# Optimization experiments

Measured on AMD Instinct MI355X. Metric: run time of the kernel, lower is better.

## Reference

```python
import jax, jax.numpy as jnp
import numpy as np

B, M, N = 16, 128, 256
USER_DIM, ANT_DIM, EDGE_DIM = 8, 2, 1
HIDDEN, HEADS = 128, 4
HD = HIDDEN // HEADS
WB, DMIN, HZ, PMAX = 2.0, 0.01, 10.0, 1.0
SCALE = 1.0 / float(np.sqrt(HD))
NEG = 0.2  # leaky relu slope


def leaky(x):
    return jnp.where(x >= 0, x, NEG * x)


def ln(x, g, b, eps=1e-5):
    m = jnp.mean(x, axis=-1, keepdims=True)
    v = jnp.mean((x - m) ** 2, axis=-1, keepdims=True)
    return (x - m) * jax.lax.rsqrt(v + eps) * g + b


def setup_inputs() -> dict:
    key = jax.random.key(0)
    ks = jax.random.split(key, 16)
    rn = lambda k, shape, s: jax.random.normal(k, shape, jnp.float32) * s
    inp = {
        "user_feats": jax.random.normal(ks[0], (B, M, USER_DIM), jnp.float32),
        "ant_feats": jax.random.uniform(ks[1], (B, N, ANT_DIM), jnp.float32),
        "edge_feats": jax.random.uniform(ks[2], (B, M, N, EDGE_DIM), jnp.float32),
        # per-head projections (Linear no-bias) + their LayerNorm affine params
        "Wu": rn(ks[3], (HEADS, HD, USER_DIM), 0.5),
        "ln_u_g": jnp.ones((HEADS, HD)), "ln_u_b": jnp.zeros((HEADS, HD)),
        "Wa": rn(ks[4], (HEADS, HD, ANT_DIM), 0.5),
        "ln_a_g": jnp.ones((HEADS, HD)), "ln_a_b": jnp.zeros((HEADS, HD)),
        "We": rn(ks[5], (HEADS, HD, EDGE_DIM), 0.5),
        "ln_e_g": jnp.ones((HEADS, HD)), "ln_e_b": jnp.zeros((HEADS, HD)),
        "attn_v": rn(ks[6], (HEADS, HD), 0.5),
        # residual proj for antennas (the user residual branch is dead code in the block)
        "Wra": rn(ks[7], (HIDDEN, ANT_DIM), 0.5), "bra": jnp.zeros((HIDDEN,)),
        "ln_ant_g": jnp.ones((HIDDEN,)), "ln_ant_b": jnp.zeros((HIDDEN,)),
        # mlp_ant
        "Wm1": rn(ks[8], (HIDDEN // 2, HIDDEN), 0.1), "bm1": jnp.full((HIDDEN // 2,), 0.1),
        "Wm2": rn(ks[9], (2, HIDDEN // 2), 0.1), "bm2": jnp.full((2,), 0.1),
        # readouts over antenna axis
        "Wd1": rn(ks[10], (2 * N, N), 0.05), "bd1": jnp.zeros((2 * N,)),
        "Wd2": rn(ks[11], (N, 2 * N), 0.05), "bd2": jnp.zeros((N,)),
        "Wp1": rn(ks[12], (2 * N, N), 0.05), "bp1": jnp.zeros((2 * N,)),
        "Wp2": rn(ks[13], (N, 2 * N), 0.05), "bp2": jnp.zeros((N,)),
    }
    return inp


def reference(user_feats, ant_feats, edge_feats, Wu, ln_u_g, ln_u_b, Wa, ln_a_g, ln_a_b,
              We, ln_e_g, ln_e_b, attn_v, Wra, bra, ln_ant_g, ln_ant_b,
              Wm1, bm1, Wm2, bm2, Wd1, bd1, Wd2, bd2, Wp1, bp1, Wp2, bp2):
    # --- per-head bipartite attention (all heads batched on axis h) ---
    U = leaky(ln(jnp.einsum('bmi,hdi->hbmd', user_feats, Wu), ln_u_g[:, None, None, :], ln_u_b[:, None, None, :]))  # [h,B,M,hd]
    A = leaky(ln(jnp.einsum('bni,hdi->hbnd', ant_feats, Wa), ln_a_g[:, None, None, :], ln_a_b[:, None, None, :]))   # [h,B,N,hd]
    E = leaky(ln(jnp.einsum('bmni,hdi->hbmnd', edge_feats, We), ln_e_g[:, None, None, None, :], ln_e_b[:, None, None, None, :]))  # [h,B,M,N,hd]
    inter = leaky(U[:, :, :, None, :] + A[:, :, None, :, :] + E)                # [h,B,M,N,hd]
    scores = jnp.einsum('hbmnd,hd->hbmn', inter, attn_v) * SCALE
    alpha = jax.nn.softmax(scores, axis=-1)                                      # max-subtract softmax over N
    ant_out = jnp.einsum('hbmd,hbmn->hbnd', U, alpha)                            # [h,B,N,hd]
    ant_cat = jnp.transpose(ant_out, (1, 2, 0, 3)).reshape(B, N, HIDDEN)         # concat heads
    a_attn = jax.nn.relu(ant_cat + leaky(ant_feats @ Wra.T + bra))
    # --- block readouts ---
    a_attn = ln(a_attn, ln_ant_g, ln_ant_b)
    h1 = jax.nn.relu(a_attn @ Wm1.T + bm1)
    ant2d = jnp.clip(jax.nn.relu(h1 @ Wm2.T + bm2), -200.0, 200.0)               # [B,N,2]
    rd = jax.nn.relu(ant2d[..., 0] @ Wd1.T + bd1) @ Wd2.T + bd2                  # [B,N]
    rp = jax.nn.relu(ant2d[..., 1] @ Wp1.T + bp1) @ Wp2.T + bp2                  # [B,N]
    rd = jnp.clip(rd, 0.0, 100.0)
    rp = jnp.nan_to_num(rp, nan=0.0, posinf=1.0, neginf=0.0)
    # delta path
    Bmax = 2.0 * WB - (N - 1) * DMIN
    da = jax.nn.relu(rd)
    sd = jnp.sum(da, axis=1, keepdims=True)
    sdelta = jnp.clip((Bmax / jnp.maximum(Bmax, sd)) * da, 0.0, 100.0)
    idx = jnp.arange(N, dtype=sdelta.dtype)
    # closed form of the sequential recurrence x[n] = x[n-1] + sdelta[n] + DMIN - WB
    x = jnp.cumsum(sdelta, axis=1) + idx * DMIN - (idx + 1.0) * WB
    positions = jnp.stack([x, jnp.zeros_like(x), jnp.full_like(x, HZ)], axis=-1)  # [B,N,3]
    # power path
    eps = 1e-3
    pa = jnp.clip(jnp.nan_to_num(jax.nn.relu(rp), nan=0.0, posinf=1.0, neginf=0.0), 0.0, 1.0)
    sp = jnp.nan_to_num(jnp.sum(pa, axis=1, keepdims=True), nan=eps, posinf=eps, neginf=-eps)
    denom = jnp.maximum(sp, eps)
    sfp = jax.lax.stop_gradient(jnp.nan_to_num(PMAX / denom, nan=1.0, posinf=1.0, neginf=0.0))
    spow = jnp.clip(jnp.nan_to_num(sfp * pa, nan=0.0, posinf=1.0, neginf=0.0), 0.0, 1.0)
    ant_feats_out = jnp.stack([sdelta, spow], axis=-1)                            # [B,N,2]
    diff = user_feats[..., :2][:, :, None, :] - positions[:, None, :, :2]         # [B,M,N,2]
    edge_feats_new = jnp.sqrt(jnp.sum(diff * diff, axis=-1, keepdims=True))       # [B,M,N,1]
    return (ant_feats_out, edge_feats_new, positions)
```

## Files before the change

### kernel.cpp

```cpp
#include <hip/hip_runtime.h>
#include <math.h>

#define H_   4
#define HD_  32
#define B_   16
#define M_   128
#define N_   256
#define MC_  16
#define MCH_ 8
#define SCALE_ 0.17677669529663687f

__device__ __forceinline__ float lrelu_f(float x) { return x >= 0.f ? x : 0.2f * x; }

__global__ __launch_bounds__(256) void k2_attn(
    const float* __restrict__ uf, const float* __restrict__ af,
    const float* __restrict__ edge,
    const float* __restrict__ Wu, const float* __restrict__ gu, const float* __restrict__ bu,
    const float* __restrict__ Wa, const float* __restrict__ ga, const float* __restrict__ ba,
    const float* __restrict__ We, const float* __restrict__ ge, const float* __restrict__ be,
    const float* __restrict__ av, float* __restrict__ P)
{
  int blk = blockIdx.x;
  int h = blk & 3, b = (blk >> 2) & 15, mc = blk >> 6;
  int tid = threadIdx.x, n = tid;
  int lane = tid & 63, wid = tid >> 6;
  __shared__ float AB[N_ * 33];
  __shared__ float4 Ut4[HD_][2];
  __shared__ float4 cbv[HD_];
  __shared__ float wred[2][MCH_][4];
  __shared__ float vw_s;

  if (tid < 32) {
    int d = tid;
    float w = We[h * HD_ + d];
    float s = w;
    #pragma unroll
    for (int o = 16; o > 0; o >>= 1) s += __shfl_xor(s, o, 32);
    float mw = s * (1.f / 32.f);
    float df = w - mw;
    float v2 = df * df;
    #pragma unroll
    for (int o = 16; o > 0; o >>= 1) v2 += __shfl_xor(v2, o, 32);
    if (d == 0) vw_s = v2 * (1.f / 32.f);
    float vv = av[h * HD_ + d] * SCALE_;
    cbv[d] = make_float4(df * ge[h * HD_ + d], be[h * HD_ + d], 0.6f * vv, 0.4f * vv);
  }
  int m0 = mc * MCH_;
  if (tid < 128) {
    int m_loc = tid >> 4, s = tid & 15, dd = s * 2;
    const float* urow = uf + (size_t)(b * M_ + m0 + m_loc) * 8;
    const float* w0 = Wu + (h * HD_ + dd) * 8;
    float x0 = 0.f, x1 = 0.f;
    #pragma unroll
    for (int i = 0; i < 8; ++i) { float u = urow[i]; x0 = fmaf(u, w0[i], x0); x1 = fmaf(u, w0[8 + i], x1); }
    float sm = x0 + x1;
    #pragma unroll
    for (int o = 8; o > 0; o >>= 1) sm += __shfl_xor(sm, o, 64);
    float mean = sm * (1.f / 32.f);
    float d0 = x0 - mean, d1 = x1 - mean;
    float vv = fmaf(d0, d0, d1 * d1);
    #pragma unroll
    for (int o = 8; o > 0; o >>= 1) vv += __shfl_xor(vv, o, 64);
    float rs = rsqrtf(vv * (1.f / 32.f) + 1e-5f);
    float y0 = fmaf(d0 * rs, gu[h * HD_ + dd],     bu[h * HD_ + dd]);
    float y1 = fmaf(d1 * rs, gu[h * HD_ + dd + 1], bu[h * HD_ + dd + 1]);
    ((float*)Ut4)[dd * MCH_ + m_loc]       = lrelu_f(y0);
    ((float*)Ut4)[(dd + 1) * MCH_ + m_loc] = lrelu_f(y1);
  }
  {
    float a0 = af[(b * N_ + n) * 2 + 0], a1 = af[(b * N_ + n) * 2 + 1];
    float ar[HD_]; float sm = 0.f;
    #pragma unroll
    for (int d = 0; d < HD_; ++d) {
      ar[d] = fmaf(a0, Wa[(h * HD_ + d) * 2], a1 * Wa[(h * HD_ + d) * 2 + 1]);
      sm += ar[d];
    }
    float mean = sm * (1.f / 32.f); float vv = 0.f;
    #pragma unroll
    for (int d = 0; d < HD_; ++d) { ar[d] -= mean; vv = fmaf(ar[d], ar[d], vv); }
    float rs = rsqrtf(vv * (1.f / 32.f) + 1e-5f);
    #pragma unroll
    for (int d = 0; d < HD_; ++d)
      AB[n * 33 + d] = lrelu_f(fmaf(ar[d] * rs, ga[h * HD_ + d], ba[h * HD_ + d]));
  }
  __syncthreads();
  float vw = vw_s;
  float tm[MCH_];
  #pragma unroll
  for (int mm = 0; mm < MCH_; ++mm) {
    float e = edge[(size_t)(b * M_ + m0 + mm) * N_ + n];
    tm[mm] = e * rsqrtf(fmaf(e * e, vw, 1e-5f));
  }
  float sc[MCH_];
  #pragma unroll
  for (int mm = 0; mm < MCH_; ++mm) sc[mm] = 0.f;
  const float* arow = &AB[n * 33];
  for (int d = 0; d < HD_; ++d) {
    float ad = arow[d];
    float4 qc = cbv[d];
    float4 u0 = Ut4[d][0], u1 = Ut4[d][1];
#define STEP(mi, uval) { float w_ = fmaf(tm[mi], qc.x, qc.y); \
    float E_ = fmaf(0.4f, fabsf(w_), 0.6f * w_); \
    float x_ = ad + uval + E_; \
    sc[mi] = fmaf(qc.z, x_, fmaf(qc.w, fabsf(x_), sc[mi])); }
    STEP(0, u0.x)  STEP(1, u0.y)  STEP(2, u0.z)  STEP(3, u0.w)
    STEP(4, u1.x)  STEP(5, u1.y)  STEP(6, u1.z)  STEP(7, u1.w)
#undef STEP
  }
  #pragma unroll
  for (int mm = 0; mm < MCH_; ++mm) {
    float v = sc[mm];
    #pragma unroll
    for (int o = 32; o > 0; o >>= 1) v = fmaxf(v, __shfl_xor(v, o, 64));
    if (lane == 0) wred[0][mm][wid] = v;
  }
  __syncthreads();
  #pragma unroll
  for (int mm = 0; mm < MCH_; ++mm) {
    float mx = fmaxf(fmaxf(wred[0][mm][0], wred[0][mm][1]),
                     fmaxf(wred[0][mm][2], wred[0][mm][3]));
    float em = __expf(sc[mm] - mx);
    sc[mm] = em;
    float ss = em;
    #pragma unroll
    for (int o = 32; o > 0; o >>= 1) ss += __shfl_xor(ss, o, 64);
    if (lane == 0) wred[1][mm][wid] = ss;
  }
  __syncthreads();
  #pragma unroll
  for (int mm = 0; mm < MCH_; ++mm) {
    float tot = (wred[1][mm][0] + wred[1][mm][1]) + (wred[1][mm][2] + wred[1][mm][3]);
    sc[mm] = sc[mm] / tot;
  }
  __syncthreads();
  float* accr = &AB[n * 33];
  for (int d = 0; d < HD_; ++d) {
    float4 u0 = Ut4[d][0], u1 = Ut4[d][1];
    float a0 = 0.f;
    a0 = fmaf(sc[0], u0.x, a0);  a0 = fmaf(sc[1], u0.y, a0);
    a0 = fmaf(sc[2], u0.z, a0);  a0 = fmaf(sc[3], u0.w, a0);
    a0 = fmaf(sc[4], u1.x, a0);  a0 = fmaf(sc[5], u1.y, a0);
    a0 = fmaf(sc[6], u1.z, a0);  a0 = fmaf(sc[7], u1.w, a0);
    accr[d] = a0;
  }
  __syncthreads();
  float* Pbase = P + (size_t)((mc * 4 + h) * B_ + b) * (N_ * HD_);
  for (int i = tid; i < N_ * HD_; i += 256) {
    int nn = i >> 5, d = i & 31;
    Pbase[i] = AB[nn * 33 + d];
  }
}

__global__ __launch_bounds__(256) void k3_mlp(
    const float* __restrict__ P, const float* __restrict__ af,
    const float* __restrict__ Wra, const float* __restrict__ bra,
    const float* __restrict__ gant, const float* __restrict__ bant,
    const float* __restrict__ Wm1, const float* __restrict__ bm1,
    const float* __restrict__ Wm2, const float* __restrict__ bm2,
    float* __restrict__ rd_in, float* __restrict__ rp_in)
{
  int b = blockIdx.x >> 4, nt = blockIdx.x & 15;
  int tid = threadIdx.x;
  int n_loc = tid >> 4, s = tid & 15;
  int n = nt * 16 + n_loc;
  int jj0 = s * 8;
  int hh = s >> 2, d0 = (s & 3) * 8;
  __shared__ float Wm1s[64][128];
  __shared__ float a2s[16][128];
  __shared__ float h1s[16][64];

  {
    const float4* wg = (const float4*)Wm1;
    float4* wl = (float4*)Wm1s;
    #pragma unroll
    for (int k = 0; k < 8; ++k) wl[tid + 256 * k] = wg[tid + 256 * k];
  }
  float cat[8];
  #pragma unroll
  for (int k = 0; k < 8; ++k) cat[k] = 0.f;
  #pragma unroll
  for (int mc = 0; mc < MC_; ++mc) {
    const float* base = P + (size_t)((mc * 4 + hh) * B_ + b) * (N_ * HD_) + n * HD_ + d0;
    float4 p0 = ((const float4*)base)[0], p1 = ((const float4*)base)[1];
    cat[0] += p0.x; cat[1] += p0.y; cat[2] += p0.z; cat[3] += p0.w;
    cat[4] += p1.x; cat[5] += p1.y; cat[6] += p1.z; cat[7] += p1.w;
  }
  float af0 = af[(b * N_ + n) * 2 + 0], af1 = af[(b * N_ + n) * 2 + 1];
  float a1[8]; float sm = 0.f;
  #pragma unroll
  for (int k = 0; k < 8; ++k) {
    int jj = jj0 + k;
    float r = fmaf(Wra[jj * 2], af0, fmaf(Wra[jj * 2 + 1], af1, bra[jj]));
    a1[k] = fmaxf(cat[k] + lrelu_f(r), 0.f);
    sm += a1[k];
  }
  #pragma unroll
  for (int o = 8; o > 0; o >>= 1) sm += __shfl_xor(sm, o, 64);
  float mean = sm * (1.f / 128.f);
  float vv = 0.f;
  #pragma unroll
  for (int k = 0; k < 8; ++k) { a1[k] -= mean; vv = fmaf(a1[k], a1[k], vv); }
  #pragma unroll
  for (int o = 8; o > 0; o >>= 1) vv += __shfl_xor(vv, o, 64);
  float rs = rsqrtf(vv * (1.f / 128.f) + 1e-5f);
  #pragma unroll
  for (int k = 0; k < 8; ++k) {
    int jj = jj0 + k;
    a2s[n_loc][jj] = fmaf(a1[k] * rs, gant[jj], bant[jj]);
  }
  __syncthreads();
  #pragma unroll
  for (int k = 0; k < 4; ++k) {
    int o = tid + 256 * k;
    int row = o & 63, nl = o >> 6;
    const float4* wr = (const float4*)Wm1s[row];
    const float4* xr = (const float4*)a2s[nl];
    float c0 = 0.f, c1 = 0.f, c2 = 0.f, c3 = 0.f;
    #pragma unroll
    for (int c = 0; c < 32; ++c) {
      int cc = (c + row) & 31;
      float4 w = wr[cc], x = xr[cc];
      c0 = fmaf(w.x, x.x, c0); c1 = fmaf(w.y, x.y, c1);
      c2 = fmaf(w.z, x.z, c2); c3 = fmaf(w.w, x.w, c3);
    }
    h1s[nl][row] = fmaxf((c0 + c1) + (c2 + c3) + bm1[row], 0.f);
  }
  __syncthreads();
  {
    int c = s >> 3, e0 = (s & 7) * 8;
    float p = 0.f;
    #pragma unroll
    for (int k = 0; k < 8; ++k) p = fmaf(h1s[n_loc][e0 + k], Wm2[c * 64 + e0 + k], p);
    #pragma unroll
    for (int o = 4; o > 0; o >>= 1) p += __shfl_xor(p, o, 64);
    if ((s & 7) == 0) {
      float v = p + bm2[c];
      v = fminf(fmaxf(v, 0.f), 200.f);
      (c == 0 ? rd_in : rp_in)[b * N_ + n] = v;
    }
  }
}

__global__ __launch_bounds__(256) void k4a_l1(
    const float* __restrict__ rd_in, const float* __restrict__ rp_in,
    const float* __restrict__ Wd1, const float* __restrict__ bd1,
    const float* __restrict__ Wp1, const float* __restrict__ bp1,
    float* __restrict__ d1buf)
{
  int r = blockIdx.x * 4 + (threadIdx.x >> 6);
  int lane = threadIdx.x & 63;
  int path = r >> 13;
  int rem = r & 8191;
  int b = rem >> 9, i = rem & 511;
  const float* W = (path ? Wp1 : Wd1) + (size_t)i * N_;
  const float* bias = path ? bp1 : bd1;
  const float* x = (path ? rp_in : rd_in) + b * N_;
  float4 w = ((const float4*)W)[lane];
  float4 xv = ((const float4*)x)[lane];
  float s = fmaf(w.x, xv.x, fmaf(w.y, xv.y, fmaf(w.z, xv.z, w.w * xv.w)));
  #pragma unroll
  for (int o = 32; o > 0; o >>= 1) s += __shfl_xor(s, o, 64);
  if (lane == 0) d1buf[r] = fmaxf(s + bias[i], 0.f);
}

__global__ __launch_bounds__(256) void k4b_l2(
    const float* __restrict__ d1buf,
    const float* __restrict__ Wd2, const float* __restrict__ bd2,
    const float* __restrict__ Wp2, const float* __restrict__ bp2,
    float* __restrict__ rdbuf, float* __restrict__ rpbuf)
{
  int r = blockIdx.x * 4 + (threadIdx.x >> 6);
  int lane = threadIdx.x & 63;
  int path = r >> 12;
  int rem = r & 4095;
  int b = rem >> 8, n = rem & 255;
  const float* W = (path ? Wp2 : Wd2) + (size_t)n * (2 * N_);
  const float* x = d1buf + path * (B_ * 2 * N_) + b * (2 * N_);
  float4 w0 = ((const float4*)W)[lane * 2], w1 = ((const float4*)W)[lane * 2 + 1];
  float4 x0 = ((const float4*)x)[lane * 2], x1 = ((const float4*)x)[lane * 2 + 1];
  float s = fmaf(w0.x, x0.x, fmaf(w0.y, x0.y, fmaf(w0.z, x0.z, w0.w * x0.w)));
  s = fmaf(w1.x, x1.x, fmaf(w1.y, x1.y, fmaf(w1.z, x1.z, fmaf(w1.w, x1.w, s))));
  #pragma unroll
  for (int o = 32; o > 0; o >>= 1) s += __shfl_xor(s, o, 64);
  if (lane == 0) {
    if (path == 0) {
      float rd = s + bd2[n];
      rd = fminf(fmaxf(rd, 0.f), 100.f);
      rdbuf[b * N_ + n] = rd;
    } else {
      float rp = s + bp2[n];
      if (isnan(rp)) rp = 0.f;
      else if (isinf(rp)) rp = rp > 0.f ? 1.f : 0.f;
      float pa = fminf(fmaxf(rp, 0.f), 1.f);
      rpbuf[b * N_ + n] = pa;
    }
  }
}

__global__ __launch_bounds__(256) void k4c_final(
    const float* __restrict__ rdbuf, const float* __restrict__ rpbuf,
    const float* __restrict__ uf,
    float* __restrict__ out_af, float* __restrict__ out_pos, float* __restrict__ out_edge)
{
  int b = blockIdx.x >> 4, g = blockIdx.x & 15;
  int q = threadIdx.x;
  int lane = q & 63, wid = q >> 6;
  __shared__ float red[8];
  float rd = rdbuf[b * N_ + q];
  float pa = rpbuf[b * N_ + q];
  float s = rd, s2 = pa;
  #pragma unroll
  for (int o = 32; o > 0; o >>= 1) { s += __shfl_xor(s, o, 64); s2 += __shfl_xor(s2, o, 64); }
  if (lane == 0) { red[wid] = s; red[4 + wid] = s2; }
  __syncthreads();
  float sd = red[0] + red[1] + red[2] + red[3];
  float sp = red[4] + red[5] + red[6] + red[7];
  const float Bmax = 2.f * 2.0f - (N_ - 1) * 0.01f;
  float f = Bmax / fmaxf(Bmax, sd);
  float sdelta = fminf(fmaxf(f * rd, 0.f), 100.f);
  float sfp = 1.0f / fmaxf(sp, 1e-3f);
  float spow = fminf(sfp * pa, 1.f);
  float val = sdelta;
  #pragma unroll
  for (int o = 1; o < 64; o <<= 1) {
    float t = __shfl_up(val, o, 64);
    if (lane >= o) val += t;
  }
  __syncthreads();
  if (lane == 63) red[wid] = val;
  __syncthreads();
  float off = 0.f;
  #pragma unroll
  for (int w2 = 0; w2 < 4; ++w2) if (w2 < wid) off += red[w2];
  float x = val + off + (float)q * 0.01f - (float)(q + 1) * 2.0f;
  if (g == 0) {
    out_af[(b * N_ + q) * 2 + 0] = sdelta;
    out_af[(b * N_ + q) * 2 + 1] = spow;
    out_pos[(b * N_ + q) * 3 + 0] = x;
    out_pos[(b * N_ + q) * 3 + 1] = 0.f;
    out_pos[(b * N_ + q) * 3 + 2] = 10.0f;
  }
  #pragma unroll
  for (int k = 0; k < 8; ++k) {
    int m = g * 8 + k;
    float u0 = uf[(b * M_ + m) * 8 + 0], u1 = uf[(b * M_ + m) * 8 + 1];
    float dx = u0 - x;
    out_edge[(size_t)(b * M_ + m) * N_ + q] = sqrtf(fmaf(dx, dx, u1 * u1));
  }
}

extern "C" void kernel_launch(void* const* d_in, const int* in_sizes, int n_in,
                              void* d_out, int out_size, void* d_ws, size_t ws_size,
                              hipStream_t stream) {
  (void)in_sizes; (void)n_in; (void)out_size; (void)ws_size;
  const float* uf   = (const float*)d_in[0];
  const float* af   = (const float*)d_in[1];
  const float* edge = (const float*)d_in[2];
  const float* Wu   = (const float*)d_in[3];
  const float* gu   = (const float*)d_in[4];
  const float* bu   = (const float*)d_in[5];
  const float* Wa   = (const float*)d_in[6];
  const float* ga   = (const float*)d_in[7];
  const float* ba   = (const float*)d_in[8];
  const float* We   = (const float*)d_in[9];
  const float* ge   = (const float*)d_in[10];
  const float* be   = (const float*)d_in[11];
  const float* av   = (const float*)d_in[12];
  const float* Wra  = (const float*)d_in[13];
  const float* bra  = (const float*)d_in[14];
  const float* gant = (const float*)d_in[15];
  const float* bant = (const float*)d_in[16];
  const float* Wm1  = (const float*)d_in[17];
  const float* bm1  = (const float*)d_in[18];
  const float* Wm2  = (const float*)d_in[19];
  const float* bm2  = (const float*)d_in[20];
  const float* Wd1  = (const float*)d_in[21];
  const float* bd1  = (const float*)d_in[22];
  const float* Wd2  = (const float*)d_in[23];
  const float* bd2  = (const float*)d_in[24];
  const float* Wp1  = (const float*)d_in[25];
  const float* bp1  = (const float*)d_in[26];
  const float* Wp2  = (const float*)d_in[27];
  const float* bp2  = (const float*)d_in[28];

  float* ws    = (float*)d_ws;
  float* P     = ws;
  float* rd_in = ws + 8388608;
  float* rp_in = ws + 8392704;
  float* d1buf = ws + 8396800;
  float* rdbuf = ws + 8413184;
  float* rpbuf = ws + 8417280;

  float* out      = (float*)d_out;
  float* out_af   = out;
  float* out_edge = out + 8192;
  float* out_pos  = out + 532480;

  hipLaunchKernelGGL(k2_attn, dim3(1024), dim3(256), 0, stream,
                     uf, af, edge, Wu, gu, bu, Wa, ga, ba, We, ge, be, av, P);
  hipLaunchKernelGGL(k3_mlp, dim3(256), dim3(256), 0, stream,
                     P, af, Wra, bra, gant, bant, Wm1, bm1, Wm2, bm2, rd_in, rp_in);
  hipLaunchKernelGGL(k4a_l1, dim3(4096), dim3(256), 0, stream,
                     rd_in, rp_in, Wd1, bd1, Wp1, bp1, d1buf);
  hipLaunchKernelGGL(k4b_l2, dim3(2048), dim3(256), 0, stream,
                     d1buf, Wd2, bd2, Wp2, bp2, rdbuf, rpbuf);
  hipLaunchKernelGGL(k4c_final, dim3(256), dim3(256), 0, stream,
                     rdbuf, rpbuf, uf, out_af, out_pos, out_edge);
}
```

Baseline: 170.6 us.

## Use packed fp16 math in attention scoring and store intermediate P as fp16

The attention kernel's score and value-aggregation loops now use packed half2 FMAs, with a partial float accumulation every 8 dims. The per-head partial output buffer P is written and read in fp16 instead of fp32, halving that intermediate traffic between the attention and MLP kernels. Shared memory layouts are reorganized into fp16 arrays. This lowers ALU and memory cost in exchange for reduced precision in the softmax logits and the accumulated outputs.

```diff
diff --git a/kernel.cpp b/kernel.cpp
--- a/kernel.cpp
+++ b/kernel.cpp
@@ -1,4 +1,5 @@
 #include <hip/hip_runtime.h>
+#include <hip/hip_fp16.h>
 #include <math.h>
 
 #define H_   4
@@ -12,21 +13,32 @@
 
 __device__ __forceinline__ float lrelu_f(float x) { return x >= 0.f ? x : 0.2f * x; }
 
+__device__ __forceinline__ __half2 u2h_(unsigned u) {
+  union { unsigned u; __half2 h; } c; c.u = u; return c.h;
+}
+__device__ __forceinline__ __half2 habs2_(__half2 x) {
+  union { __half2 h; unsigned u; } c; c.h = x; c.u &= 0x7FFF7FFFu; return c.h;
+}
+__device__ __forceinline__ unsigned splat2_(float f) {
+  unsigned short s = __half_as_ushort(__float2half(f));
+  return (unsigned)s | ((unsigned)s << 16);
+}
+
 __global__ __launch_bounds__(256) void k2_attn(
     const float* __restrict__ uf, const float* __restrict__ af,
     const float* __restrict__ edge,
     const float* __restrict__ Wu, const float* __restrict__ gu, const float* __restrict__ bu,
     const float* __restrict__ Wa, const float* __restrict__ ga, const float* __restrict__ ba,
     const float* __restrict__ We, const float* __restrict__ ge, const float* __restrict__ be,
-    const float* __restrict__ av, float* __restrict__ P)
+    const float* __restrict__ av, unsigned short* __restrict__ P)
 {
   int blk = blockIdx.x;
   int h = blk & 3, b = (blk >> 2) & 15, mc = blk >> 6;
   int tid = threadIdx.x, n = tid;
   int lane = tid & 63, wid = tid >> 6;
-  __shared__ float AB[N_ * 33];
-  __shared__ float4 Ut4[HD_][2];
-  __shared__ float4 cbv[HD_];
+  __shared__ __align__(16) unsigned short As[HD_ * N_];
+  __shared__ __align__(16) unsigned short accs[N_ * 34];
+  __shared__ __align__(16) unsigned short rows[HD_ * 16];
   __shared__ float wred[2][MCH_][4];
   __shared__ float vw_s;
 
@@ -42,8 +54,13 @@
     #pragma unroll
     for (int o = 16; o > 0; o >>= 1) v2 += __shfl_xor(v2, o, 32);
     if (d == 0) vw_s = v2 * (1.f / 32.f);
-    float vv = av[h * HD_ + d] * SCALE_;
-    cbv[d] = make_float4(df * ge[h * HD_ + d], be[h * HD_ + d], 0.6f * vv, 0.4f * vv);
+    float vvf = av[h * HD_ + d] * SCALE_;
+    uint4 t;
+    t.x = splat2_(df * ge[h * HD_ + d]);
+    t.y = splat2_(be[h * HD_ + d]);
+    t.z = splat2_(0.6f * vvf);
+    t.w = splat2_(0.4f * vvf);
+    *(uint4*)&rows[d * 16 + 8] = t;
   }
   int m0 = mc * MCH_;
   if (tid < 128) {
@@ -64,8 +81,8 @@
     float rs = rsqrtf(vv * (1.f / 32.f) + 1e-5f);
     float y0 = fmaf(d0 * rs, gu[h * HD_ + dd],     bu[h * HD_ + dd]);
     float y1 = fmaf(d1 * rs, gu[h * HD_ + dd + 1], bu[h * HD_ + dd + 1]);
-    ((float*)Ut4)[dd * MCH_ + m_loc]       = lrelu_f(y0);
-    ((float*)Ut4)[(dd + 1) * MCH_ + m_loc] = lrelu_f(y1);
+    rows[dd * 16 + m_loc]       = __half_as_ushort(__float2half(lrelu_f(y0)));
+    rows[(dd + 1) * 16 + m_loc] = __half_as_ushort(__float2half(lrelu_f(y1)));
   }
   {
     float a0 = af[(b * N_ + n) * 2 + 0], a1 = af[(b * N_ + n) * 2 + 1];
@@ -81,35 +98,54 @@
     float rs = rsqrtf(vv * (1.f / 32.f) + 1e-5f);
     #pragma unroll
     for (int d = 0; d < HD_; ++d)
-      AB[n * 33 + d] = lrelu_f(fmaf(ar[d] * rs, ga[h * HD_ + d], ba[h * HD_ + d]));
+      As[d * N_ + n] = __half_as_ushort(__float2half(
+          lrelu_f(fmaf(ar[d] * rs, ga[h * HD_ + d], ba[h * HD_ + d]))));
   }
   __syncthreads();
   float vw = vw_s;
-  float tm[MCH_];
+  float tmf[MCH_];
   #pragma unroll
   for (int mm = 0; mm < MCH_; ++mm) {
     float e = edge[(size_t)(b * M_ + m0 + mm) * N_ + n];
-    tm[mm] = e * rsqrtf(fmaf(e * e, vw, 1e-5f));
-  }
-  float sc[MCH_];
-  #pragma unroll
-  for (int mm = 0; mm < MCH_; ++mm) sc[mm] = 0.f;
-  const float* arow = &AB[n * 33];
-  for (int d = 0; d < HD_; ++d) {
-    float ad = arow[d];
-    float4 qc = cbv[d];
-    float4 u0 = Ut4[d][0], u1 = Ut4[d][1];
-#define STEP(mi, uval) { float w_ = fmaf(tm[mi], qc.x, qc.y); \
-    float E_ = fmaf(0.4f, fabsf(w_), 0.6f * w_); \
-    float x_ = ad + uval + E_; \
-    sc[mi] = fmaf(qc.z, x_, fmaf(qc.w, fabsf(x_), sc[mi])); }
-    STEP(0, u0.x)  STEP(1, u0.y)  STEP(2, u0.z)  STEP(3, u0.w)
-    STEP(4, u1.x)  STEP(5, u1.y)  STEP(6, u1.z)  STEP(7, u1.w)
-#undef STEP
+    tmf[mm] = e * rsqrtf(fmaf(e * e, vw, 1e-5f));
+  }
+  __half2 tm2[4];
+  #pragma unroll
+  for (int j = 0; j < 4; ++j) tm2[j] = __floats2half2_rn(tmf[2 * j], tmf[2 * j + 1]);
+  const __half2 hz = __float2half2_rn(0.f);
+  const __half2 c06 = __float2half2_rn(0.6f), c04 = __float2half2_rn(0.4f);
+  float scF[MCH_];
+  #pragma unroll
+  for (int mm = 0; mm < MCH_; ++mm) scF[mm] = 0.f;
+  __half2 sc2[4] = {hz, hz, hz, hz};
+  #pragma unroll
+  for (int dc = 0; dc < 4; ++dc) {
+    #pragma unroll
+    for (int dk = 0; dk < 8; ++dk) {
+      int d = dc * 8 + dk;
+      __half2 ad2 = __half2half2(__ushort_as_half(As[d * N_ + n]));
+      uint4 ru = *(const uint4*)&rows[d * 16];
+      uint4 rc = *(const uint4*)&rows[d * 16 + 8];
+      __half2 cc = u2h_(rc.x), bb = u2h_(rc.y), vz = u2h_(rc.z), vw2 = u2h_(rc.w);
+      unsigned ruv[4] = {ru.x, ru.y, ru.z, ru.w};
+      #pragma unroll
+      for (int j = 0; j < 4; ++j) {
+        __half2 w2 = __hfma2(tm2[j], cc, bb);
+        __half2 adu = __hadd2(ad2, u2h_(ruv[j]));
+        __half2 x2 = __hfma2(c06, w2, __hfma2(c04, habs2_(w2), adu));
+        sc2[j] = __hfma2(vz, x2, __hfma2(vw2, habs2_(x2), sc2[j]));
+      }
+    }
+    #pragma unroll
+    for (int j = 0; j < 4; ++j) {
+      float2 f = __half22float2(sc2[j]);
+      scF[2 * j] += f.x; scF[2 * j + 1] += f.y;
+      sc2[j] = hz;
+    }
   }
   #pragma unroll
   for (int mm = 0; mm < MCH_; ++mm) {
-    float v = sc[mm];
+    float v = scF[mm];
     #pragma unroll
     for (int o = 32; o > 0; o >>= 1) v = fmaxf(v, __shfl_xor(v, o, 64));
     if (lane == 0) wred[0][mm][wid] = v;
@@ -119,8 +155,8 @@
   for (int mm = 0; mm < MCH_; ++mm) {
     float mx = fmaxf(fmaxf(wred[0][mm][0], wred[0][mm][1]),
                      fmaxf(wred[0][mm][2], wred[0][mm][3]));
-    float em = __expf(sc[mm] - mx);
-    sc[mm] = em;
+    float em = __expf(scF[mm] - mx);
+    scF[mm] = em;
     float ss = em;
     #pragma unroll
     for (int o = 32; o > 0; o >>= 1) ss += __shfl_xor(ss, o, 64);
@@ -130,29 +166,33 @@
   #pragma unroll
   for (int mm = 0; mm < MCH_; ++mm) {
     float tot = (wred[1][mm][0] + wred[1][mm][1]) + (wred[1][mm][2] + wred[1][mm][3]);
-    sc[mm] = sc[mm] / tot;
-  }
-  __syncthreads();
-  float* accr = &AB[n * 33];
+    scF[mm] = scF[mm] / tot;
+  }
+  __half2 al2[4];
+  #pragma unroll
+  for (int j = 0; j < 4; ++j) al2[j] = __floats2half2_rn(scF[2 * j], scF[2 * j + 1]);
+  #pragma unroll 8
   for (int d = 0; d < HD_; ++d) {
-    float4 u0 = Ut4[d][0], u1 = Ut4[d][1];
-    float a0 = 0.f;
-    a0 = fmaf(sc[0], u0.x, a0);  a0 = fmaf(sc[1], u0.y, a0);
-    a0 = fmaf(sc[2], u0.z, a0);  a0 = fmaf(sc[3], u0.w, a0);
-    a0 = fmaf(sc[4], u1.x, a0);  a0 = fmaf(sc[5], u1.y, a0);
-    a0 = fmaf(sc[6], u1.z, a0);  a0 = fmaf(sc[7], u1.w, a0);
-    accr[d] = a0;
-  }
-  __syncthreads();
-  float* Pbase = P + (size_t)((mc * 4 + h) * B_ + b) * (N_ * HD_);
-  for (int i = tid; i < N_ * HD_; i += 256) {
-    int nn = i >> 5, d = i & 31;
-    Pbase[i] = AB[nn * 33 + d];
+    uint4 ru = *(const uint4*)&rows[d * 16];
+    unsigned ruv[4] = {ru.x, ru.y, ru.z, ru.w};
+    __half2 pv = hz;
+    #pragma unroll
+    for (int j = 0; j < 4; ++j) pv = __hfma2(al2[j], u2h_(ruv[j]), pv);
+    float2 pf = __half22float2(pv);
+    accs[n * 34 + d] = __half_as_ushort(__float2half(pf.x + pf.y));
+  }
+  __syncthreads();
+  unsigned short* Pbase = P + (size_t)((mc * 4 + h) * B_ + b) * (N_ * HD_);
+  #pragma unroll
+  for (int k = 0; k < 16; ++k) {
+    int i = tid + 256 * k;
+    int nn = i >> 4, dp = i & 15;
+    *(unsigned*)&Pbase[nn * 32 + dp * 2] = *(const unsigned*)&accs[nn * 34 + dp * 2];
   }
 }
 
 __global__ __launch_bounds__(256) void k3_mlp(
-    const float* __restrict__ P, const float* __restrict__ af,
+    const unsigned short* __restrict__ P, const float* __restrict__ af,
     const float* __restrict__ Wra, const float* __restrict__ bra,
     const float* __restrict__ gant, const float* __restrict__ bant,
     const float* __restrict__ Wm1, const float* __restrict__ bm1,
@@ -180,10 +220,13 @@
   for (int k = 0; k < 8; ++k) cat[k] = 0.f;
   #pragma unroll
   for (int mc = 0; mc < MC_; ++mc) {
-    const float* base = P + (size_t)((mc * 4 + hh) * B_ + b) * (N_ * HD_) + n * HD_ + d0;
-    float4 p0 = ((const float4*)base)[0], p1 = ((const float4*)base)[1];
-    cat[0] += p0.x; cat[1] += p0.y; cat[2] += p0.z; cat[3] += p0.w;
-    cat[4] += p1.x; cat[5] += p1.y; cat[6] += p1.z; cat[7] += p1.w;
+    const unsigned short* base = P + (size_t)((mc * 4 + hh) * B_ + b) * (N_ * HD_) + n * HD_ + d0;
+    uint4 p = *(const uint4*)base;
+    float2 f;
+    f = __half22float2(u2h_(p.x)); cat[0] += f.x; cat[1] += f.y;
+    f = __half22float2(u2h_(p.y)); cat[2] += f.x; cat[3] += f.y;
+    f = __half22float2(u2h_(p.z)); cat[4] += f.x; cat[5] += f.y;
+    f = __half22float2(u2h_(p.w)); cat[6] += f.x; cat[7] += f.y;
   }
   float af0 = af[(b * N_ + n) * 2 + 0], af1 = af[(b * N_ + n) * 2 + 1];
   float a1[8]; float sm = 0.f;
@@ -384,12 +427,12 @@
   const float* bp2  = (const float*)d_in[28];
 
   float* ws    = (float*)d_ws;
-  float* P     = ws;
-  float* rd_in = ws + 8388608;
-  float* rp_in = ws + 8392704;
-  float* d1buf = ws + 8396800;
-  float* rdbuf = ws + 8413184;
-  float* rpbuf = ws + 8417280;
+  unsigned short* P = (unsigned short*)d_ws;
+  float* rd_in = ws + 4194304;
+  float* rp_in = ws + 4198400;
+  float* d1buf = ws + 4202496;
+  float* rdbuf = ws + 4218880;
+  float* rpbuf = ws + 4222976;
 
   float* out      = (float*)d_out;
   float* out_af   = out;
```

Result: slower. 189.3 us (+11.0%).
